# Performance work log

Measured on AMD Instinct MI355X. Metric: run time of the kernel, lower is better.

## Reference

```python
import jax, jax.numpy as jnp
import numpy as np

DT = 0.1       # time separation between grid points (forward dt arg default)
UT = 0.1       # stationary-mode time constant
K_IN, K_OUT, K_STATE = 8, 4, 128
PRE_LEN, FWD_LEN, BATCH = 64, 128, 4096


def setup_inputs() -> dict:
    key = jax.random.key(0)
    ks = jax.random.split(key, 16)
    H = K_STATE
    s = 0.05  # small init keeps the 128-step integration numerically tame
    d = {}
    d['pre_x'] = jax.random.normal(ks[0], (PRE_LEN, BATCH, K_IN), jnp.float32)
    d['pre_y'] = jax.random.normal(ks[1], (PRE_LEN, BATCH, K_OUT), jnp.float32)
    d['forward_x'] = jax.random.normal(ks[2], (FWD_LEN, BATCH, K_IN), jnp.float32)
    # encoder nn.GRU (1 layer), torch gate order r,z,n
    d['W_ih'] = jax.random.normal(ks[3], (3 * H, K_IN + K_OUT), jnp.float32) * s
    d['W_hh'] = jax.random.normal(ks[4], (3 * H, H), jnp.float32) * s
    d['b_ih'] = jax.random.normal(ks[5], (3 * H,), jnp.float32) * s
    d['b_hh'] = jax.random.normal(ks[6], (3 * H,), jnp.float32) * s
    # expand_input: Linear(k_in, k_state) + Tanh
    d['W_e'] = jax.random.normal(ks[7], (H, K_IN), jnp.float32) * s
    d['b_e'] = jax.random.normal(ks[8], (H,), jnp.float32) * s
    # ODE GRU cell (BasicCell with net_type='GRU'): input size = k_state
    d['Wc_ih'] = jax.random.normal(ks[9], (3 * H, H), jnp.float32) * s
    d['Wc_hh'] = jax.random.normal(ks[10], (3 * H, H), jnp.float32) * s
    d['bc_ih'] = jax.random.normal(ks[11], (3 * H,), jnp.float32) * s
    d['bc_hh'] = jax.random.normal(ks[12], (3 * H,), jnp.float32) * s
    # fc: Linear(H, 2H, bias=False) -> Tanh -> Linear(2H, k_out, bias=False)
    d['W1'] = jax.random.normal(ks[13], (2 * H, H), jnp.float32) * s
    d['W2'] = jax.random.normal(ks[14], (K_OUT, 2 * H), jnp.float32) * s
    return d


def _gru_cell(x, h, Wi, Wh, bi, bh):
    gi = x @ Wi.T + bi
    gh = h @ Wh.T + bh
    ir, iz, inn = jnp.split(gi, 3, axis=-1)
    hr, hz, hn = jnp.split(gh, 3, axis=-1)
    r = jax.nn.sigmoid(ir + hr)
    z = jax.nn.sigmoid(iz + hz)
    n = jnp.tanh(inn + r * hn)
    return (1.0 - z) * n + z * h


def reference(pre_x, pre_y, forward_x, W_ih, W_hh, b_ih, b_hh, W_e, b_e,
              Wc_ih, Wc_hh, bc_ih, bc_hh, W1, W2):
    H = W_hh.shape[1]
    # ---- GRU encoder over [pre_x, pre_y], take final hidden state ----
    enc_in = jnp.concatenate([pre_x, pre_y], axis=2)  # [Tp, B, k_in+k_out]
    h0 = jnp.zeros((enc_in.shape[1], H), enc_in.dtype)

    def enc_step(h, x):
        return _gru_cell(x, h, W_ih, W_hh, b_ih, b_hh), None

    hn, _ = jax.lax.scan(enc_step, h0, enc_in)  # [B, H]

    # ---- natural cubic spline of the control input over the grid ----
    L = forward_x.shape[0]
    hs = DT
    ys = jnp.concatenate([pre_x[-1:], forward_x], axis=0)  # [L+1, B, k_in]
    rhs = 6.0 * (ys[:-2] - 2.0 * ys[1:-1] + ys[2:]) / (hs * hs)  # [L-1, ...]
    nin = L - 1
    A = 4.0 * jnp.eye(nin) + jnp.eye(nin, k=1) + jnp.eye(nin, k=-1)
    Minner = jnp.linalg.solve(A, rhs.reshape(nin, -1)).reshape(rhs.shape)
    zpad = jnp.zeros_like(ys[:1])
    M = jnp.concatenate([zpad, Minner, zpad], axis=0)  # 2nd derivs, [L+1,B,k_in]

    def u(t):
        i = jnp.clip(jnp.floor(t / hs).astype(jnp.int32), 0, L - 1)
        t0 = i.astype(ys.dtype) * hs
        a = (t0 + hs - t) / hs
        b = (t - t0) / hs
        yi, yi1 = jnp.take(ys, i, axis=0), jnp.take(ys, i + 1, axis=0)
        Mi, Mi1 = jnp.take(M, i, axis=0), jnp.take(M, i + 1, axis=0)
        return a * yi + b * yi1 + ((a ** 3 - a) * Mi + (b ** 3 - b) * Mi1) * (hs * hs) / 6.0

    # ---- ODE system: stationary GRU-cell dynamics ----
    def f(t, y):
        x = jnp.tanh(u(t) @ W_e.T + b_e)
        return (_gru_cell(x, y, Wc_ih, Wc_hh, bc_ih, bc_hh) - y) / UT

    # ---- fixed-grid RK4 (torchdiffeq method='rk4', one step per interval) ----
    def rk4(y, t0):
        k1 = f(t0, y)
        k2 = f(t0 + hs / 2, y + (hs / 2) * k1)
        k3 = f(t0 + hs / 2, y + (hs / 2) * k2)
        k4 = f(t0 + hs, y + hs * k3)
        yn = y + (hs / 6.0) * (k1 + 2 * k2 + 2 * k3 + k4)
        return yn, yn

    t_starts = jnp.arange(L, dtype=ys.dtype) * hs
    _, traj = jax.lax.scan(rk4, hn, t_starts)  # [L, B, H]

    # ---- output head: Linear -> Tanh -> Linear (no bias) ----
    return jnp.tanh(traj @ W1.T) @ W2.T  # [L, B, k_out]
```

## Files before the change

### kernel.cpp

```cpp
#include <hip/hip_runtime.h>
#include <math.h>

#define NB    4096
#define NH    128
#define NKIN  8
#define NKOUT 4
#define NTP   64
#define NL    128
#define BKIN  (NB*NKIN)
#define LOG2E 1.44269504088896340736f

typedef __attribute__((ext_vector_type(8))) short short8;
typedef __attribute__((ext_vector_type(4))) float f32x4;

#if __has_builtin(__builtin_amdgcn_exp2f)
#define EXP2F __builtin_amdgcn_exp2f
#else
#define EXP2F exp2f
#endif

__device__ __forceinline__ short f2bf(float f) {
    union { float f; unsigned u; } v; v.f = f;
    unsigned u = v.u;
    return (short)((u + 0x7fffu + ((u >> 16) & 1u)) >> 16);
}
__device__ __forceinline__ unsigned pkbf2(float a, float b) {
#if __has_builtin(__builtin_amdgcn_cvt_pk_bf16_f32)
    auto p = __builtin_amdgcn_cvt_pk_bf16_f32(a, b);
    unsigned q; __builtin_memcpy(&q, &p, 4); return q;
#else
    union { float f; unsigned u; } x, y; x.f = a; y.f = b;
    unsigned ua = (x.u + 0x7fffu + ((x.u >> 16) & 1u)) >> 16;
    unsigned ub = (y.u + 0x7fffu + ((y.u >> 16) & 1u)) & 0xffff0000u;
    return ua | ub;
#endif
}
__device__ __forceinline__ void st4(short* dst, const f32x4& v) {
    uint2 q; q.x = pkbf2(v[0], v[1]); q.y = pkbf2(v[2], v[3]);
    *(uint2*)dst = q;
}
__device__ __forceinline__ f32x4 exp24(f32x4 a) {
    f32x4 r;
    #pragma unroll
    for (int i = 0; i < 4; ++i) r[i] = EXP2F(a[i]);
    return r;
}
__device__ __forceinline__ f32x4 rcp4(f32x4 a) {
    f32x4 r;
    #pragma unroll
    for (int i = 0; i < 4; ++i) r[i] = __builtin_amdgcn_rcpf(a[i]);
    return r;
}

__global__ void spline_um_kernel(const float* __restrict__ pre_x,
                                 const float* __restrict__ fx,
                                 float* __restrict__ UM)
{
    __shared__ float cp[128];
    if (threadIdx.x == 0) {
        float c = 0.f;
        for (int j = 1; j <= 127; ++j) { c = 1.0f/(4.0f - c); cp[j] = c; }
    }
    __syncthreads();
    int col = blockIdx.x*128 + threadIdx.x;
    const float r6 = 6.0f/(0.1f*0.1f);
    const float KK = 0.01f/16.0f;
    float y0 = pre_x[(size_t)(NTP-1)*BKIN + col];
    float y1 = fx[col];
    float d = 0.f;
    for (int j = 1; j <= 127; ++j) {
        float y2 = fx[(size_t)j*BKIN + col];
        float r  = r6*(y0 - 2.f*y1 + y2);
        d = (r - d)*cp[j];
        UM[(size_t)j*BKIN + col] = d;
        y0 = y1; y1 = y2;
    }
    float xn  = 0.f;
    float yj1 = fx[(size_t)127*BKIN + col];
    for (int j = 127; j >= 1; --j) {
        float dj = UM[(size_t)j*BKIN + col];
        float x  = dj - cp[j]*xn;
        float yj = fx[(size_t)(j-1)*BKIN + col];
        UM[(size_t)j*BKIN + col] = 0.5f*(yj + yj1) - KK*(x + xn);
        xn = x; yj1 = yj;
    }
    float ys0 = pre_x[(size_t)(NTP-1)*BKIN + col];
    UM[col] = 0.5f*(ys0 + yj1) - KK*xn;
}

__global__ void prep_frags(const float* __restrict__ W1, const float* __restrict__ W2,
                           short* __restrict__ w1f, short* __restrict__ w2f)
{
    int tid = threadIdx.x;
    for (int idx = tid; idx < 16*4*64*8; idx += 256) {
        int j = idx & 7, lane = (idx >> 3) & 63, kc = (idx >> 9) & 3, t = idx >> 11;
        int row = t*16 + (lane & 15);
        int k   = kc*32 + (lane >> 4)*8 + j;
        w1f[idx] = f2bf(2.0f*LOG2E*W1[row*NH + k]);
    }
    for (int idx = tid; idx < 8*64*8; idx += 256) {
        int j = idx & 7, lane = (idx >> 3) & 63, kc = idx >> 9;
        int m = lane & 15;
        int k = kc*32 + (lane >> 4)*8 + j;
        w2f[idx] = (m < NKOUT) ? f2bf(W2[m*2*NH + k]) : (short)0;
    }
}

__device__ __forceinline__ void ld4(const short* bp, short8 (&bf)[4]) {
    #pragma unroll
    for (int kc = 0; kc < 4; ++kc) bf[kc] = *(const short8*)(bp + kc*32);
}
__device__ __forceinline__ void gemmR(const short8 (&bf)[4], const short8 (&A)[3][4],
                                      f32x4 (&acc)[3]) {
    #pragma unroll
    for (int kc = 0; kc < 4; ++kc)
        #pragma unroll
        for (int g = 0; g < 3; ++g)
            acc[g] = __builtin_amdgcn_mfma_f32_16x16x32_bf16(A[g][kc], bf[kc], acc[g], 0, 0, 0);
}
__device__ __forceinline__ void gemmB(const short* bp, const short8 (&A)[3][4], f32x4 (&acc)[3]) {
    short8 bf[4]; ld4(bp, bf); gemmR(bf, A, acc);
}
__device__ __forceinline__ void gateK(const f32x4 (&gi)[3], const f32x4 (&gh)[3],
                                      const f32x4& yin, f32x4& K)
{
    f32x4 rg = rcp4(exp24(gi[0] + gh[0]) + 1.0f);
    f32x4 zc = rcp4(exp24(gi[1] + gh[1]) + 1.0f);
    f32x4 tg = 1.0f - 2.0f*rcp4(exp24(gi[2] + rg*gh[2]) + 1.0f);
    K = zc*(tg - yin);
}

__global__ void __launch_bounds__(512, 2)
fused_kernel(const float* __restrict__ pre_x, const float* __restrict__ pre_y,
             const float* __restrict__ fx,
             const float* __restrict__ W_ih, const float* __restrict__ W_hh,
             const float* __restrict__ b_ih, const float* __restrict__ b_hh,
             const float* __restrict__ W_e,  const float* __restrict__ b_e,
             const float* __restrict__ Wc_ih,const float* __restrict__ Wc_hh,
             const float* __restrict__ bc_ih,const float* __restrict__ bc_hh,
             const float* __restrict__ UM,   const short* __restrict__ w1f,
             const short* __restrict__ w2f,  float* __restrict__ out)
{
    __shared__ __align__(16) short yTa[16*136];
    __shared__ __align__(16) short yTb[16*136];
    __shared__ __align__(16) short E1 [16*136];
    __shared__ __align__(16) short xmT[16*136];
    __shared__ __align__(16) short x1T[16*136];
    __shared__ __align__(16) short UMb[16*40];
    __shared__ __align__(16) short U1b[16*40];
    __shared__ __align__(16) short oT [16*264];

    const int tid  = threadIdx.x;
    const int w    = tid >> 6;
    const int lane = tid & 63;
    const int quad = lane >> 4;
    const int m    = lane & 15;
    const int hq   = w*16 + quad*4;
    const int b0   = blockIdx.x * 16;
    const f32x4 z4 = {0.f, 0.f, 0.f, 0.f};
    const float scg[3] = {-LOG2E, LOG2E, 2.0f*LOG2E};

    for (int i = tid; i < 16*136; i += 512) yTa[i] = 0;
    for (int i = tid; i < 16*40;  i += 512) { UMb[i] = 0; U1b[i] = 0; }

    f32x4 y = z4;

    {
        short8 Ehh[3][4];
        #pragma unroll
        for (int g = 0; g < 3; ++g)
            #pragma unroll
            for (int c = 0; c < 4; ++c) {
                const float* ph = W_hh + (size_t)(g*NH + w*16 + m)*NH + c*32 + quad*8;
                short8 fh;
                #pragma unroll
                for (int j = 0; j < 8; ++j) fh[j] = f2bf(scg[g]*ph[j]);
                Ehh[g][c] = fh;
            }
        short8 Eih[3];
        #pragma unroll
        for (int g = 0; g < 3; ++g) {
            short8 f1;
            #pragma unroll
            for (int j = 0; j < 8; ++j) {
                int k = quad*8 + j;
                f1[j] = (k < 12) ? f2bf(scg[g]*W_ih[(size_t)(g*NH + w*16 + m)*12 + k]) : (short)0;
            }
            Eih[g] = f1;
        }
        f32x4 erz4, ezz4, egn4, ein4;
        #pragma unroll
        for (int r = 0; r < 4; ++r) {
            int h = hq + r;
            erz4[r] = -LOG2E*(b_ih[h]      + b_hh[h]);
            ezz4[r] =  LOG2E*(b_ih[NH + h] + b_hh[NH + h]);
            egn4[r] = 2.0f*LOG2E*b_hh[2*NH + h];
            ein4[r] = 2.0f*LOG2E*b_ih[2*NH + h];
        }
        const int eidx = w*24 + lane;
        const int eb = eidx/12, ek = eidx - 12*eb;
        const bool estg = (lane < 24);
        float encv = 0.f;
        if (estg) {
            float e0 = (ek < NKIN) ? pre_x[((size_t)0*NB + b0 + eb)*NKIN + ek]
                                   : pre_y[((size_t)0*NB + b0 + eb)*NKOUT + (ek - NKIN)];
            UMb[eb*40 + ek] = f2bf(e0);
            encv = (ek < NKIN) ? pre_x[((size_t)1*NB + b0 + eb)*NKIN + ek]
                               : pre_y[((size_t)1*NB + b0 + eb)*NKOUT + (ek - NKIN)];
        }
        __syncthreads();
        for (int t = 0; t < NTP; ++t) {
            float evn = 0.f;
            if (estg) {
                int tn = (t + 2 < NTP) ? t + 2 : NTP - 1;
                evn = (ek < NKIN) ? pre_x[((size_t)tn*NB + b0 + eb)*NKIN + ek]
                                  : pre_y[((size_t)tn*NB + b0 + eb)*NKOUT + (ek - NKIN)];
            }
            const short* bin_buf  = (t & 1) ? U1b : UMb;
            short*       bout_buf = (t & 1) ? UMb : U1b;
            const short* sin_buf  = (t & 1) ? yTb : yTa;
            short*       sout_buf = (t & 1) ? yTa : yTb;
            f32x4 gi[3] = {z4, z4, ein4};
            {
                short8 b = *(const short8*)(bin_buf + m*40 + quad*8);
                #pragma unroll
                for (int g = 0; g < 3; ++g)
                    gi[g] = __builtin_amdgcn_mfma_f32_16x16x32_bf16(Eih[g], b, gi[g], 0, 0, 0);
            }
            f32x4 gh[3] = {erz4, ezz4, egn4};
            gemmB(sin_buf + m*136 + quad*8, Ehh, gh);
            f32x4 K;
            gateK(gi, gh, y, K);
            y += K;
            st4(sout_buf + m*136 + hq, y);
            if (estg) { bout_buf[eb*40 + ek] = f2bf(encv); encv = evn; }
            __syncthreads();
        }
    }

    short8 Ahh[3][4], Aih[3][4];
    #pragma unroll
    for (int g = 0; g < 3; ++g)
        #pragma unroll
        for (int c = 0; c < 4; ++c) {
            const float* ph = Wc_hh + (size_t)(g*NH + w*16 + m)*NH + c*32 + quad*8;
            const float* pi = Wc_ih + (size_t)(g*NH + w*16 + m)*NH + c*32 + quad*8;
            short8 fh, fi;
            #pragma unroll
            for (int j = 0; j < 8; ++j) { fh[j] = f2bf(scg[g]*ph[j]); fi[j] = f2bf(scg[g]*pi[j]); }
            Ahh[g][c] = fh; Aih[g][c] = fi;
        }
    short8 Aexp;
    #pragma unroll
    for (int j = 0; j < 8; ++j) {
        int k = quad*8 + j;
        Aexp[j] = (k < NKIN) ? f2bf(2.0f*LOG2E*W_e[(w*16 + m)*NKIN + k]) : (short)0;
    }
    short8 A1f[2][4];
    #pragma unroll
    for (int kc = 0; kc < 4; ++kc) {
        A1f[0][kc] = *(const short8*)(w1f + (size_t)(((w    )*4 + kc)*64 + lane)*8);
        A1f[1][kc] = *(const short8*)(w1f + (size_t)(((w + 8)*4 + kc)*64 + lane)*8);
    }
    f32x4 brz4, bzz4, bgn4, bin4, be4;
    #pragma unroll
    for (int r = 0; r < 4; ++r) {
        int h = hq + r;
        brz4[r] = -LOG2E*(bc_ih[h]      + bc_hh[h]);
        bzz4[r] =  LOG2E*(bc_ih[NH + h] + bc_hh[NH + h]);
        bgn4[r] = 2.0f*LOG2E*bc_hh[2*NH + h];
        bin4[r] = 2.0f*LOG2E*bc_ih[2*NH + h];
        be4[r]  = 2.0f*LOG2E*b_e[h];
    }

    const bool stg = (lane < 16);
    const int sb = w*2 + (lane >> 3), sk = lane & 7;
    const size_t scol = (size_t)(b0 + sb)*NKIN + sk;
    if (stg) {
        UMb[sb*40 + 8 + (lane & 3)] = 0;
        U1b[sb*40 + 8 + (lane & 3)] = 0;
        UMb[sb*40 + sk] = f2bf(pre_x[(size_t)(NTP-1)*BKIN + scol]);
    }
    __syncthreads();
    {
        short8 b = *(const short8*)(UMb + m*40 + quad*8);
        f32x4 c0 = be4;
        c0 = __builtin_amdgcn_mfma_f32_16x16x32_bf16(Aexp, b, c0, 0, 0, 0);
        f32x4 xv = 1.0f - 2.0f*rcp4(exp24(c0) + 1.0f);
        st4(xmT + m*136 + hq, xv);
    }
    __syncthreads();
    f32x4 gi0[3] = {z4, z4, bin4};
    gemmB(xmT + m*136 + quad*8, Aih, gi0);
    if (stg) { UMb[sb*40 + sk] = f2bf(UM[scol]); U1b[sb*40 + sk] = f2bf(fx[scol]); }
    __syncthreads();
    {
        short8 bm = *(const short8*)(UMb + m*40 + quad*8);
        short8 b1 = *(const short8*)(U1b + m*40 + quad*8);
        f32x4 cm = be4, c1 = be4;
        cm = __builtin_amdgcn_mfma_f32_16x16x32_bf16(Aexp, bm, cm, 0, 0, 0);
        c1 = __builtin_amdgcn_mfma_f32_16x16x32_bf16(Aexp, b1, c1, 0, 0, 0);
        f32x4 xm = 1.0f - 2.0f*rcp4(exp24(cm) + 1.0f);
        f32x4 x1 = 1.0f - 2.0f*rcp4(exp24(c1) + 1.0f);
        st4(xmT + m*136 + hq, xm);
        st4(x1T + m*136 + hq, x1);
    }
    float fxv = 0.f, umv = 0.f;
    if (stg) { fxv = fx[(size_t)BKIN + scol]; umv = UM[(size_t)BKIN + scol]; }
    __syncthreads();

    for (int st = 0; st < NL; ++st) {
        short8 byf[4];
        ld4(yTa + m*136 + quad*8, byf);
        f32x4 gh[3] = {brz4, bzz4, bgn4};
        gemmR(byf, Ahh, gh);
        f32x4 gim[3] = {z4, z4, bin4};
        gemmB(xmT + m*136 + quad*8, Aih, gim);
        f32x4 K, Ks, ye;
        gateK(gi0, gh, y, K);
        Ks = K; ye = y + 0.5f*K;
        st4(yTb + m*136 + hq, ye);
        __syncthreads();
        if (stg) { UMb[sb*40 + sk] = f2bf(umv); U1b[sb*40 + sk] = f2bf(fxv); }
        gh[0] = brz4; gh[1] = bzz4; gh[2] = bgn4;
        gemmB(yTb + m*136 + quad*8, Ahh, gh);
        if (st > 0) {
            f32x4 o0 = z4, o1 = z4;
            #pragma unroll
            for (int kc = 0; kc < 4; ++kc) {
                o0 = __builtin_amdgcn_mfma_f32_16x16x32_bf16(A1f[0][kc], byf[kc], o0, 0, 0, 0);
                o1 = __builtin_amdgcn_mfma_f32_16x16x32_bf16(A1f[1][kc], byf[kc], o1, 0, 0, 0);
            }
            f32x4 t0 = 1.0f - 2.0f*rcp4(exp24(o0) + 1.0f);
            f32x4 t1 = 1.0f - 2.0f*rcp4(exp24(o1) + 1.0f);
            st4(oT + m*264 + w*16     + quad*4, t0);
            st4(oT + m*264 + (w+8)*16 + quad*4, t1);
        }
        gateK(gim, gh, ye, K);
        Ks += 2.0f*K; ye = y + 0.5f*K;
        st4(E1 + m*136 + hq, ye);
        __syncthreads();
        if (stg) {
            int sn = (st + 2 < NL) ? st + 2 : NL - 1;
            fxv = fx[(size_t)sn*BKIN + scol];
            umv = UM[(size_t)sn*BKIN + scol];
        }
        gh[0] = brz4; gh[1] = bzz4; gh[2] = bgn4;
        gemmB(E1 + m*136 + quad*8, Ahh, gh);
        f32x4 gi1[3] = {z4, z4, bin4};
        gemmB(x1T + m*136 + quad*8, Aih, gi1);
        gateK(gim, gh, ye, K);
        Ks += 2.0f*K; ye = y + K;
        st4(yTb + m*136 + hq, ye);
        __syncthreads();
        short8 a2f[8];
        const bool s2w = (st > 0) && (w == ((st-1) & 7));
        if (s2w) {
            #pragma unroll
            for (int kc = 0; kc < 8; ++kc)
                a2f[kc] = *(const short8*)(w2f + (size_t)(kc*64 + lane)*8);
        }
        gh[0] = brz4; gh[1] = bzz4; gh[2] = bgn4;
        gemmB(yTb + m*136 + quad*8, Ahh, gh);
        {
            short8 bm = *(const short8*)(UMb + m*40 + quad*8);
            short8 b1 = *(const short8*)(U1b + m*40 + quad*8);
            f32x4 cm = be4, c1 = be4;
            cm = __builtin_amdgcn_mfma_f32_16x16x32_bf16(Aexp, bm, cm, 0, 0, 0);
            c1 = __builtin_amdgcn_mfma_f32_16x16x32_bf16(Aexp, b1, c1, 0, 0, 0);
            f32x4 xm = 1.0f - 2.0f*rcp4(exp24(cm) + 1.0f);
            f32x4 x1 = 1.0f - 2.0f*rcp4(exp24(c1) + 1.0f);
            st4(xmT + m*136 + hq, xm);
            st4(x1T + m*136 + hq, x1);
        }
        if (s2w) {
            f32x4 oc = z4;
            #pragma unroll
            for (int kc = 0; kc < 8; ++kc) {
                short8 b = *(const short8*)(oT + m*264 + kc*32 + quad*8);
                oc = __builtin_amdgcn_mfma_f32_16x16x32_bf16(a2f[kc], b, oc, 0, 0, 0);
            }
            if (quad == 0)
                *(f32x4*)(out + ((size_t)(st-1)*NB + b0 + m)*NKOUT) = oc;
        }
        gateK(gi1, gh, ye, K);
        y += (1.0f/6.0f)*(Ks + K);
        st4(yTa + m*136 + hq, y);
        gi0[0] = gi1[0]; gi0[1] = gi1[1]; gi0[2] = gi1[2];
        __syncthreads();
    }

    {
        short8 byf[4];
        ld4(yTa + m*136 + quad*8, byf);
        f32x4 o0 = z4, o1 = z4;
        #pragma unroll
        for (int kc = 0; kc < 4; ++kc) {
            o0 = __builtin_amdgcn_mfma_f32_16x16x32_bf16(A1f[0][kc], byf[kc], o0, 0, 0, 0);
            o1 = __builtin_amdgcn_mfma_f32_16x16x32_bf16(A1f[1][kc], byf[kc], o1, 0, 0, 0);
        }
        f32x4 t0 = 1.0f - 2.0f*rcp4(exp24(o0) + 1.0f);
        f32x4 t1 = 1.0f - 2.0f*rcp4(exp24(o1) + 1.0f);
        st4(oT + m*264 + w*16     + quad*4, t0);
        st4(oT + m*264 + (w+8)*16 + quad*4, t1);
        short8 a2f[8];
        if (w == 7) {
            #pragma unroll
            for (int kc = 0; kc < 8; ++kc)
                a2f[kc] = *(const short8*)(w2f + (size_t)(kc*64 + lane)*8);
        }
        __syncthreads();
        if (w == 7) {
            f32x4 oc = z4;
            #pragma unroll
            for (int kc = 0; kc < 8; ++kc) {
                short8 b = *(const short8*)(oT + m*264 + kc*32 + quad*8);
                oc = __builtin_amdgcn_mfma_f32_16x16x32_bf16(a2f[kc], b, oc, 0, 0, 0);
            }
            if (quad == 0)
                *(f32x4*)(out + ((size_t)(NL-1)*NB + b0 + m)*NKOUT) = oc;
        }
    }
}

extern "C" void kernel_launch(void* const* d_in, const int* in_sizes, int n_in,
                              void* d_out, int out_size, void* d_ws, size_t ws_size,
                              hipStream_t stream)
{
    const float* pre_x = (const float*)d_in[0];
    const float* pre_y = (const float*)d_in[1];
    const float* fx    = (const float*)d_in[2];
    const float* W_ih  = (const float*)d_in[3];
    const float* W_hh  = (const float*)d_in[4];
    const float* b_ih  = (const float*)d_in[5];
    const float* b_hh  = (const float*)d_in[6];
    const float* W_e   = (const float*)d_in[7];
    const float* b_e   = (const float*)d_in[8];
    const float* Wc_ih = (const float*)d_in[9];
    const float* Wc_hh = (const float*)d_in[10];
    const float* bc_ih = (const float*)d_in[11];
    const float* bc_hh = (const float*)d_in[12];
    const float* W1    = (const float*)d_in[13];
    const float* W2    = (const float*)d_in[14];
    float* out = (float*)d_out;

    float* UM  = (float*)d_ws;
    short* w1f = (short*)((char*)d_ws + (size_t)NL*NB*NKIN*4);
    short* w2f = w1f + 16*4*64*8;

    prep_frags<<<dim3(1), dim3(256), 0, stream>>>(W1, W2, w1f, w2f);
    spline_um_kernel<<<dim3((NB*NKIN)/128), dim3(128), 0, stream>>>(pre_x, fx, UM);
    fused_kernel<<<dim3(NB/16), dim3(512), 0, stream>>>(
        pre_x, pre_y, fx, W_ih, W_hh, b_ih, b_hh, W_e, b_e,
        Wc_ih, Wc_hh, bc_ih, bc_hh, UM, w1f, w2f, out);
}
```

Baseline: 840.4 us.

## Fuse spline-coefficient solve into main kernel and restructure RK4 step loop

Removes the separate spline tridiagonal-solve kernel and runs the solve per block inside the fused kernel, using the 16 staging lanes and shared scratch for the recurrence coefficients. The RK4 loop is reordered so the four stages run sequentially, the output head runs at the end of each step, and the input-gate GEMMs for the next step are hoisted to the end of the iteration. prep_frags is also spread over 8 blocks. This saves a kernel launch and a global round trip, but the serial 127-step solve now sits inside the latency-bound main kernel on only 16 lanes per block, and the loop body gains an extra barrier.

```diff
diff --git a/kernel.cpp b/kernel.cpp
--- a/kernel.cpp
+++ b/kernel.cpp
@@ -52,53 +52,17 @@
     return r;
 }
 
-__global__ void spline_um_kernel(const float* __restrict__ pre_x,
-                                 const float* __restrict__ fx,
-                                 float* __restrict__ UM)
-{
-    __shared__ float cp[128];
-    if (threadIdx.x == 0) {
-        float c = 0.f;
-        for (int j = 1; j <= 127; ++j) { c = 1.0f/(4.0f - c); cp[j] = c; }
-    }
-    __syncthreads();
-    int col = blockIdx.x*128 + threadIdx.x;
-    const float r6 = 6.0f/(0.1f*0.1f);
-    const float KK = 0.01f/16.0f;
-    float y0 = pre_x[(size_t)(NTP-1)*BKIN + col];
-    float y1 = fx[col];
-    float d = 0.f;
-    for (int j = 1; j <= 127; ++j) {
-        float y2 = fx[(size_t)j*BKIN + col];
-        float r  = r6*(y0 - 2.f*y1 + y2);
-        d = (r - d)*cp[j];
-        UM[(size_t)j*BKIN + col] = d;
-        y0 = y1; y1 = y2;
-    }
-    float xn  = 0.f;
-    float yj1 = fx[(size_t)127*BKIN + col];
-    for (int j = 127; j >= 1; --j) {
-        float dj = UM[(size_t)j*BKIN + col];
-        float x  = dj - cp[j]*xn;
-        float yj = fx[(size_t)(j-1)*BKIN + col];
-        UM[(size_t)j*BKIN + col] = 0.5f*(yj + yj1) - KK*(x + xn);
-        xn = x; yj1 = yj;
-    }
-    float ys0 = pre_x[(size_t)(NTP-1)*BKIN + col];
-    UM[col] = 0.5f*(ys0 + yj1) - KK*xn;
-}
-
 __global__ void prep_frags(const float* __restrict__ W1, const float* __restrict__ W2,
                            short* __restrict__ w1f, short* __restrict__ w2f)
 {
-    int tid = threadIdx.x;
-    for (int idx = tid; idx < 16*4*64*8; idx += 256) {
+    int tid0 = blockIdx.x*256 + threadIdx.x;
+    for (int idx = tid0; idx < 16*4*64*8; idx += 8*256) {
         int j = idx & 7, lane = (idx >> 3) & 63, kc = (idx >> 9) & 3, t = idx >> 11;
         int row = t*16 + (lane & 15);
         int k   = kc*32 + (lane >> 4)*8 + j;
         w1f[idx] = f2bf(2.0f*LOG2E*W1[row*NH + k]);
     }
-    for (int idx = tid; idx < 8*64*8; idx += 256) {
+    for (int idx = tid0; idx < 8*64*8; idx += 8*256) {
         int j = idx & 7, lane = (idx >> 3) & 63, kc = idx >> 9;
         int m = lane & 15;
         int k = kc*32 + (lane >> 4)*8 + j;
@@ -138,7 +102,7 @@
              const float* __restrict__ W_e,  const float* __restrict__ b_e,
              const float* __restrict__ Wc_ih,const float* __restrict__ Wc_hh,
              const float* __restrict__ bc_ih,const float* __restrict__ bc_hh,
-             const float* __restrict__ UM,   const short* __restrict__ w1f,
+             float* __restrict__ UM,         const short* __restrict__ w1f,
              const short* __restrict__ w2f,  float* __restrict__ out)
 {
     __shared__ __align__(16) short yTa[16*136];
@@ -276,10 +240,49 @@
     const bool stg = (lane < 16);
     const int sb = w*2 + (lane >> 3), sk = lane & 7;
     const size_t scol = (size_t)(b0 + sb)*NKIN + sk;
+    float* cpS = (float*)E1;
+    float prex_last = 0.f;
+    if (stg) prex_last = pre_x[(size_t)(NTP-1)*BKIN + scol];
+    if (stg) {
+        const float r6 = 6.0f/(0.1f*0.1f);
+        float c = 0.f, d = 0.f;
+        float yp = fx[(size_t)127*BKIN + scol];
+        float y0 = fx[(size_t)126*BKIN + scol];
+        float ym = fx[(size_t)125*BKIN + scol];
+        #pragma unroll 4
+        for (int j = 127; j >= 1; --j) {
+            float r = r6*(ym - 2.f*y0 + yp);
+            c = __builtin_amdgcn_rcpf(4.f - c);
+            d = (r - d)*c;
+            UM[(size_t)j*BKIN + scol] = d;
+            if (tid == 0) cpS[128 - j] = c;
+            yp = y0; y0 = ym;
+            ym = (j >= 3) ? fx[(size_t)(j-3)*BKIN + scol] : prex_last;
+        }
+    }
+    __syncthreads();
+    if (stg) {
+        const float KK = 0.01f/16.0f;
+        float Mp = 0.f;
+        float y0 = prex_last;
+        float y1 = fx[scol];
+        #pragma unroll 4
+        for (int j = 1; j <= 127; ++j) {
+            float dj = UM[(size_t)j*BKIN + scol];
+            float e  = cpS[128 - j];
+            float Mj = dj - e*Mp;
+            UM[(size_t)(j-1)*BKIN + scol] = 0.5f*(y0 + y1) - KK*(Mp + Mj);
+            Mp = Mj; y0 = y1;
+            y1 = fx[(size_t)j*BKIN + scol];
+        }
+        UM[(size_t)127*BKIN + scol] = 0.5f*(y0 + y1) - KK*Mp;
+    }
+    __syncthreads();
+
     if (stg) {
         UMb[sb*40 + 8 + (lane & 3)] = 0;
         U1b[sb*40 + 8 + (lane & 3)] = 0;
-        UMb[sb*40 + sk] = f2bf(pre_x[(size_t)(NTP-1)*BKIN + scol]);
+        UMb[sb*40 + sk] = f2bf(prex_last);
     }
     __syncthreads();
     {
@@ -308,23 +311,45 @@
     float fxv = 0.f, umv = 0.f;
     if (stg) { fxv = fx[(size_t)BKIN + scol]; umv = UM[(size_t)BKIN + scol]; }
     __syncthreads();
+    f32x4 gim[3] = {z4, z4, bin4}, gi1[3] = {z4, z4, bin4};
+    gemmB(xmT + m*136 + quad*8, Aih, gim);
+    gemmB(x1T + m*136 + quad*8, Aih, gi1);
 
     for (int st = 0; st < NL; ++st) {
-        short8 byf[4];
-        ld4(yTa + m*136 + quad*8, byf);
         f32x4 gh[3] = {brz4, bzz4, bgn4};
-        gemmR(byf, Ahh, gh);
-        f32x4 gim[3] = {z4, z4, bin4};
-        gemmB(xmT + m*136 + quad*8, Aih, gim);
+        gemmB(yTa + m*136 + quad*8, Ahh, gh);
         f32x4 K, Ks, ye;
         gateK(gi0, gh, y, K);
         Ks = K; ye = y + 0.5f*K;
         st4(yTb + m*136 + hq, ye);
         __syncthreads();
+        gh[0] = brz4; gh[1] = bzz4; gh[2] = bgn4;
+        gemmB(yTb + m*136 + quad*8, Ahh, gh);
+        gateK(gim, gh, ye, K);
+        Ks += 2.0f*K; ye = y + 0.5f*K;
+        st4(E1 + m*136 + hq, ye);
+        __syncthreads();
+        gh[0] = brz4; gh[1] = bzz4; gh[2] = bgn4;
+        gemmB(E1 + m*136 + quad*8, Ahh, gh);
+        gateK(gim, gh, ye, K);
+        Ks += 2.0f*K; ye = y + K;
+        st4(yTb + m*136 + hq, ye);
+        __syncthreads();
         if (stg) { UMb[sb*40 + sk] = f2bf(umv); U1b[sb*40 + sk] = f2bf(fxv); }
         gh[0] = brz4; gh[1] = bzz4; gh[2] = bgn4;
         gemmB(yTb + m*136 + quad*8, Ahh, gh);
-        if (st > 0) {
+        gateK(gi1, gh, ye, K);
+        y += (1.0f/6.0f)*(Ks + K);
+        st4(yTa + m*136 + hq, y);
+        __syncthreads();
+        if (stg) {
+            int sn = (st + 2 < NL) ? st + 2 : NL - 1;
+            fxv = fx[(size_t)sn*BKIN + scol];
+            umv = UM[(size_t)sn*BKIN + scol];
+        }
+        {
+            short8 byf[4];
+            ld4(yTa + m*136 + quad*8, byf);
             f32x4 o0 = z4, o1 = z4;
             #pragma unroll
             for (int kc = 0; kc < 4; ++kc) {
@@ -336,32 +361,6 @@
             st4(oT + m*264 + w*16     + quad*4, t0);
             st4(oT + m*264 + (w+8)*16 + quad*4, t1);
         }
-        gateK(gim, gh, ye, K);
-        Ks += 2.0f*K; ye = y + 0.5f*K;
-        st4(E1 + m*136 + hq, ye);
-        __syncthreads();
-        if (stg) {
-            int sn = (st + 2 < NL) ? st + 2 : NL - 1;
-            fxv = fx[(size_t)sn*BKIN + scol];
-            umv = UM[(size_t)sn*BKIN + scol];
-        }
-        gh[0] = brz4; gh[1] = bzz4; gh[2] = bgn4;
-        gemmB(E1 + m*136 + quad*8, Ahh, gh);
-        f32x4 gi1[3] = {z4, z4, bin4};
-        gemmB(x1T + m*136 + quad*8, Aih, gi1);
-        gateK(gim, gh, ye, K);
-        Ks += 2.0f*K; ye = y + K;
-        st4(yTb + m*136 + hq, ye);
-        __syncthreads();
-        short8 a2f[8];
-        const bool s2w = (st > 0) && (w == ((st-1) & 7));
-        if (s2w) {
-            #pragma unroll
-            for (int kc = 0; kc < 8; ++kc)
-                a2f[kc] = *(const short8*)(w2f + (size_t)(kc*64 + lane)*8);
-        }
-        gh[0] = brz4; gh[1] = bzz4; gh[2] = bgn4;
-        gemmB(yTb + m*136 + quad*8, Ahh, gh);
         {
             short8 bm = *(const short8*)(UMb + m*40 + quad*8);
             short8 b1 = *(const short8*)(U1b + m*40 + quad*8);
@@ -373,7 +372,12 @@
             st4(xmT + m*136 + hq, xm);
             st4(x1T + m*136 + hq, x1);
         }
-        if (s2w) {
+        __syncthreads();
+        if (w == (st & 7)) {
+            short8 a2f[8];
+            #pragma unroll
+            for (int kc = 0; kc < 8; ++kc)
+                a2f[kc] = *(const short8*)(w2f + (size_t)(kc*64 + lane)*8);
             f32x4 oc = z4;
             #pragma unroll
             for (int kc = 0; kc < 8; ++kc) {
@@ -381,45 +385,13 @@
                 oc = __builtin_amdgcn_mfma_f32_16x16x32_bf16(a2f[kc], b, oc, 0, 0, 0);
             }
             if (quad == 0)
-                *(f32x4*)(out + ((size_t)(st-1)*NB + b0 + m)*NKOUT) = oc;
-        }
-        gateK(gi1, gh, ye, K);
-        y += (1.0f/6.0f)*(Ks + K);
-        st4(yTa + m*136 + hq, y);
+                *(f32x4*)(out + ((size_t)st*NB + b0 + m)*NKOUT) = oc;
+        }
         gi0[0] = gi1[0]; gi0[1] = gi1[1]; gi0[2] = gi1[2];
-        __syncthreads();
-    }
-
-    {
-        short8 byf[4];
-        ld4(yTa + m*136 + quad*8, byf);
-        f32x4 o0 = z4, o1 = z4;
-        #pragma unroll
-        for (int kc = 0; kc < 4; ++kc) {
-            o0 = __builtin_amdgcn_mfma_f32_16x16x32_bf16(A1f[0][kc], byf[kc], o0, 0, 0, 0);
-            o1 = __builtin_amdgcn_mfma_f32_16x16x32_bf16(A1f[1][kc], byf[kc], o1, 0, 0, 0);
-        }
-        f32x4 t0 = 1.0f - 2.0f*rcp4(exp24(o0) + 1.0f);
-        f32x4 t1 = 1.0f - 2.0f*rcp4(exp24(o1) + 1.0f);
-        st4(oT + m*264 + w*16     + quad*4, t0);
-        st4(oT + m*264 + (w+8)*16 + quad*4, t1);
-        short8 a2f[8];
-        if (w == 7) {
-            #pragma unroll
-            for (int kc = 0; kc < 8; ++kc)
-                a2f[kc] = *(const short8*)(w2f + (size_t)(kc*64 + lane)*8);
-        }
-        __syncthreads();
-        if (w == 7) {
-            f32x4 oc = z4;
-            #pragma unroll
-            for (int kc = 0; kc < 8; ++kc) {
-                short8 b = *(const short8*)(oT + m*264 + kc*32 + quad*8);
-                oc = __builtin_amdgcn_mfma_f32_16x16x32_bf16(a2f[kc], b, oc, 0, 0, 0);
-            }
-            if (quad == 0)
-                *(f32x4*)(out + ((size_t)(NL-1)*NB + b0 + m)*NKOUT) = oc;
-        }
+        gim[0] = z4; gim[1] = z4; gim[2] = bin4;
+        gi1[0] = z4; gi1[1] = z4; gi1[2] = bin4;
+        gemmB(xmT + m*136 + quad*8, Aih, gim);
+        gemmB(x1T + m*136 + quad*8, Aih, gi1);
     }
 }
 
@@ -448,8 +420,7 @@
     short* w1f = (short*)((char*)d_ws + (size_t)NL*NB*NKIN*4);
     short* w2f = w1f + 16*4*64*8;
 
-    prep_frags<<<dim3(1), dim3(256), 0, stream>>>(W1, W2, w1f, w2f);
-    spline_um_kernel<<<dim3((NB*NKIN)/128), dim3(128), 0, stream>>>(pre_x, fx, UM);
+    prep_frags<<<dim3(8), dim3(256), 0, stream>>>(W1, W2, w1f, w2f);
     fused_kernel<<<dim3(NB/16), dim3(512), 0, stream>>>(
         pre_x, pre_y, fx, W_ih, W_hh, b_ih, b_hh, W_e, b_e,
         Wc_ih, Wc_hh, bc_ih, bc_hh, UM, w1f, w2f, out);
```

New measurement: 717.1 us. 14.7% less time.
